# Optimization experiments

Measured on AMD Instinct MI355X. Metric: run time of the kernel, lower is better.

The kernel has to match this reference:

```python
import jax, jax.numpy as jnp
import numpy as np

BLK = 128          # block size for fp8 block-wise scales
FP8_MAX = 448.0    # max representable magnitude of float8_e4m3fn


def _dequant_act(a, s):
    # a: (E, M, K) fp8 values stored in fp32; s: (E, M, K//BLK) per-token 1x128 scales
    E, M, K = a.shape
    nb = K // BLK
    return (a.reshape(E, M, nb, BLK) * s[..., None]).reshape(E, M, K)


def _dequant_w(w, s):
    # w: (E, N, K) fp8 values stored in fp32; s: (E, N//BLK, K//BLK) 128x128 block scales
    E, N, K = w.shape
    return (w.reshape(E, N // BLK, BLK, K // BLK, BLK) * s[:, :, None, :, None]).reshape(E, N, K)


def _fp8_round(x):
    # round-to-fp8(e4m3fn) with straight-through value semantics
    q = x.astype(jnp.float8_e4m3fn).astype(jnp.float32)
    return x + jax.lax.stop_gradient(q - x)


def setup_inputs() -> dict:
    key = jax.random.key(0)
    ks = jax.random.split(key, 8)
    E, N, K, M = 8, 2048, 4096, 1024
    f8 = lambda x: x.astype(jnp.float8_e4m3fn).astype(jnp.float32)
    hidden_states_fp8 = f8(jax.random.normal(ks[0], (E, M, K), dtype=jnp.float32))
    hidden_states_scale = jax.random.uniform(ks[1], (E, M, K // BLK), dtype=jnp.float32, minval=0.01, maxval=1.0)
    masked_m = jax.random.randint(ks[2], (E,), 1, M + 1, dtype=jnp.int32)
    w13_weight_fp8 = f8(jax.random.normal(ks[3], (E, N, K), dtype=jnp.float32))
    w13_weight_scale = jax.random.uniform(ks[4], (E, N // BLK, K // BLK), dtype=jnp.float32, minval=0.01, maxval=1.0)
    w2_weight_fp8 = f8(jax.random.normal(ks[5], (E, K, N // 2), dtype=jnp.float32))
    w2_weight_scale = jax.random.uniform(ks[6], (E, K // BLK, N // 2 // BLK), dtype=jnp.float32, minval=0.01, maxval=1.0)
    return {
        "hidden_states_fp8": hidden_states_fp8,
        "hidden_states_scale": hidden_states_scale,
        "masked_m": masked_m,
        "expected_m": 512,
        "w13_weight_fp8": w13_weight_fp8,
        "w13_weight_scale": w13_weight_scale,
        "w2_weight_fp8": w2_weight_fp8,
        "w2_weight_scale": w2_weight_scale,
    }


def reference(hidden_states_fp8, hidden_states_scale, masked_m, expected_m,
              w13_weight_fp8, w13_weight_scale, w2_weight_fp8, w2_weight_scale):
    E, M, K = hidden_states_fp8.shape
    # per-expert row validity mask (rows >= masked_m[e] are padding)
    mask = jnp.arange(M)[None, :] < masked_m[:, None]            # (E, M)

    # --- grouped GEMM 1: (x @ w13^T) -> bf16, masked by valid rows ---
    a = _dequant_act(hidden_states_fp8, hidden_states_scale)     # (E, M, K)
    w13 = _dequant_w(w13_weight_fp8, w13_weight_scale)           # (E, N, K)
    gateup = jnp.einsum('emk,enk->emn', a, w13)
    gateup = gateup.astype(jnp.bfloat16).astype(jnp.float32)     # gemm emits bf16

    # --- fused SiLU * mul + per-128-block fp8 quantization ---
    gate, up = jnp.split(gateup, 2, axis=-1)                     # (E, M, N/2) each
    x = jax.nn.silu(gate) * up
    x = jnp.where(mask[..., None], x, 0.0)
    N2 = x.shape[-1]
    nb = N2 // BLK
    xb = x.reshape(E, M, nb, BLK)
    amax = jnp.max(jnp.abs(xb), axis=-1)                         # (E, M, nb)
    scale = jnp.maximum(amax, 1e-10) / FP8_MAX
    q = _fp8_round(xb / scale[..., None])                        # fp8-rounded values
    a2 = (q * scale[..., None]).reshape(E, M, N2)                # dequantized for gemm 2

    # --- grouped GEMM 2: (down_input @ w2^T) -> bf16 ---
    w2 = _dequant_w(w2_weight_fp8, w2_weight_scale)              # (E, K, N/2)
    out = jnp.einsum('emn,ekn->emk', a2, w2).astype(jnp.bfloat16)
    out = jnp.where(mask[..., None], out, jnp.bfloat16(0))
    return out
```

## Files before the change

kernel.cpp:

```cpp
#include <hip/hip_runtime.h>
#include <hip/hip_bf16.h>

#define E_  8
#define M_  1024
#define K_  4096
#define N_  2048
#define N2_ 1024

typedef unsigned short u16;
typedef unsigned char  u8;
typedef unsigned int   u32;
typedef long           i64;

typedef __bf16 bf16x8 __attribute__((ext_vector_type(8)));
typedef float  f32x4  __attribute__((ext_vector_type(4)));

union FragU { uint4 u; bf16x8 v; };

__device__ __forceinline__ u16 f2bfu(float f){
  union { __hip_bfloat16 h; u16 u; } c;
  c.h = __float2bfloat16(f);
  return c.u;
}
__device__ __forceinline__ u32 pack2(float a, float b){
  return (u32)f2bfu(a) | ((u32)f2bfu(b) << 16);
}
__device__ __forceinline__ float bf2f(u16 u){
  u32 x = ((u32)u) << 16;
  return __uint_as_float(x);
}
__device__ __forceinline__ float bf16val(float f){
  return bf2f(f2bfu(f));
}
__device__ __forceinline__ float fp8_round(float x){
  float ax = fabsf(x);
  if (ax < 0.015625f){
    return rintf(x * 512.0f) * (1.0f/512.0f);
  }
  u32 u = __float_as_uint(x);
  u32 lsb = (u >> 20) & 1u;
  u += 0x7FFFFu + lsb;
  u &= 0xFFF00000u;
  return __uint_as_float(u);
}
__device__ __forceinline__ u32 f2fp8(float v){
  u32 b = __float_as_uint(v);
  u32 s = (b >> 24) & 0x80u;
  int e = (int)((b >> 23) & 0xffu);
  u32 m = (b >> 20) & 7u;
  if (e >= 121) return s | ((u32)(e - 120) << 3) | m;
  return s | (u32)(fabsf(v) * 512.0f + 0.25f);
}

#define GLD16(g, l) __builtin_amdgcn_global_load_lds( \
    (const __attribute__((address_space(1))) void*)(g), \
    (__attribute__((address_space(3))) void*)(l), 16, 0, 0)

template<bool MASKED>
__global__ __launch_bounds__(256) void conv8_kernel(
    const float* __restrict__ src_, const int* __restrict__ masked_m,
    u8* __restrict__ dst)
{
  const int row = blockIdx.x, e = blockIdx.y;
  if (MASKED && row >= masked_m[e]) return;
  const int t = threadIdx.x;
  const size_t R = (size_t)e*gridDim.x + row;
  const float* s = src_ + R*K_ + t*16;
  const float4 f0 = *reinterpret_cast<const float4*>(s);
  const float4 f1 = *reinterpret_cast<const float4*>(s + 4);
  const float4 f2 = *reinterpret_cast<const float4*>(s + 8);
  const float4 f3 = *reinterpret_cast<const float4*>(s + 12);
  uint4 w;
  w.x = f2fp8(f0.x) | (f2fp8(f0.y)<<8) | (f2fp8(f0.z)<<16) | (f2fp8(f0.w)<<24);
  w.y = f2fp8(f1.x) | (f2fp8(f1.y)<<8) | (f2fp8(f1.z)<<16) | (f2fp8(f1.w)<<24);
  w.z = f2fp8(f2.x) | (f2fp8(f2.y)<<8) | (f2fp8(f2.z)<<16) | (f2fp8(f2.w)<<24);
  w.w = f2fp8(f3.x) | (f2fp8(f3.y)<<8) | (f2fp8(f3.z)<<16) | (f2fp8(f3.w)<<24);
  const int td = (t & ~7) | ((t & 7) ^ (row & 7));
  *reinterpret_cast<uint4*>(dst + R*K_ + td*16) = w;
}

__global__ __launch_bounds__(256, 2) void gemm1_fp8(
    const u8* __restrict__ A8, const float* __restrict__ Ascale,
    const u8* __restrict__ B8, const float* __restrict__ Wscale,
    const int* __restrict__ masked_m, u16* __restrict__ Cu)
{
  const int tn = blockIdx.x, tm = blockIdx.y, e = blockIdx.z;
  const int m0 = tm*128, n0 = tn*128;
  const int me = masked_m[e];
  if (m0 >= me) return;
  const int tid = threadIdx.x;
  const int lane = tid & 63, wid = tid >> 6;

  __shared__ u8 sA[2][128*128];
  __shared__ u8 sB[2][128*128];
  __shared__ float sSa[2][128];

  const size_t rbA = (size_t)e*M_ + m0;
  const size_t rbB = (size_t)e*N_ + n0;

  auto ISSUE = [&](const u8* G, size_t rowbase, int kt, u8* Sbuf){
    #pragma unroll
    for (int q = 0; q < 4; ++q){
      const int ins = wid*4 + q;
      const int r   = ins*8 + (lane >> 3);
      const u8* src = G + (rowbase + r)*K_ + kt*128 + (lane & 7)*16;
      GLD16(src, Sbuf + ins*1024);
    }
  };

  const int wm = wid >> 1, wn = wid & 1;
  const int fr = lane & 15, kg = lane >> 4;

  f32x4 acc[4][4];
  #pragma unroll
  for (int i = 0; i < 4; ++i)
    #pragma unroll
    for (int j = 0; j < 4; ++j)
      acc[i][j] = (f32x4){0.f, 0.f, 0.f, 0.f};

  float rSa = 0.f;
  if (tid < 128) rSa = Ascale[(rbA + tid)*32 + 0];
  ISSUE(A8, rbA, 0, sA[0]);
  ISSUE(B8, rbB, 0, sB[0]);
  if (tid < 128) sSa[0][tid] = rSa;
  asm volatile("s_waitcnt vmcnt(0) lgkmcnt(0)" ::: "memory");
  __builtin_amdgcn_s_barrier();
  __builtin_amdgcn_sched_barrier(0);

  int cur = 0;
  for (int kt = 0; kt < 32; ++kt){
    if (kt + 1 < 32){
      if (tid < 128) rSa = Ascale[(rbA + tid)*32 + kt + 1];
      ISSUE(A8, rbA, kt + 1, sA[cur ^ 1]);
      ISSUE(B8, rbB, kt + 1, sB[cur ^ 1]);
      if (tid < 128) sSa[cur ^ 1][tid] = rSa;
      asm volatile("s_waitcnt vmcnt(8)" ::: "memory");
    } else {
      asm volatile("s_waitcnt vmcnt(0)" ::: "memory");
    }
    __builtin_amdgcn_s_barrier();
    __builtin_amdgcn_sched_barrier(0);

    const float sw = Wscale[((size_t)e*16 + tn)*32 + kt];
    f32x4 blk[4][4];
    #pragma unroll
    for (int ks = 0; ks < 4; ++ks){
      i64 av[4], bv[4];
      #pragma unroll
      for (int i = 0; i < 4; ++i){
        const int r   = wm*64 + i*16 + fr;
        const int c16 = ks*2 + (kg >> 1);
        const int ad  = r*128 + ((c16 ^ (r & 7)) << 4) + ((kg & 1) << 3);
        av[i] = *reinterpret_cast<const i64*>(&sA[cur][ad]);
      }
      #pragma unroll
      for (int j = 0; j < 4; ++j){
        const int r   = wn*64 + j*16 + fr;
        const int c16 = ks*2 + (kg >> 1);
        const int ad  = r*128 + ((c16 ^ (r & 7)) << 4) + ((kg & 1) << 3);
        bv[j] = *reinterpret_cast<const i64*>(&sB[cur][ad]);
      }
      asm volatile("s_waitcnt lgkmcnt(0)" ::: "memory");
      __builtin_amdgcn_sched_barrier(0);
      __builtin_amdgcn_s_setprio(1);
      #pragma unroll
      for (int i = 0; i < 4; ++i)
        #pragma unroll
        for (int j = 0; j < 4; ++j){
          f32x4 cin = (ks == 0) ? (f32x4){0.f,0.f,0.f,0.f} : blk[i][j];
          blk[i][j] = __builtin_amdgcn_mfma_f32_16x16x32_fp8_fp8(av[i], bv[j], cin, 0, 0, 0);
        }
      __builtin_amdgcn_s_setprio(0);
      if (ks == 3){
        #pragma unroll
        for (int i = 0; i < 4; ++i){
          f32x4 sa = *reinterpret_cast<const f32x4*>(&sSa[cur][wm*64 + i*16 + kg*4]);
          sa *= sw;
          #pragma unroll
          for (int j = 0; j < 4; ++j)
            acc[i][j] += sa * blk[i][j];
        }
        asm volatile("s_waitcnt lgkmcnt(0)" ::: "memory");
      }
      __builtin_amdgcn_s_barrier();
    }
    cur ^= 1;
  }

  #pragma unroll
  for (int i = 0; i < 4; ++i){
    #pragma unroll
    for (int j = 0; j < 4; ++j){
      #pragma unroll
      for (int r = 0; r < 4; ++r){
        const int gm = m0 + wm*64 + i*16 + kg*4 + r;
        const int gn = n0 + wn*64 + j*16 + fr;
        if (gm < me) Cu[((size_t)e*M_ + gm)*N_ + gn] = f2bfu(acc[i][j][r]);
      }
    }
  }
}

template<int KD, int ND>
__global__ __launch_bounds__(256, 2) void gemm2_bf16(
    const u16* __restrict__ Abf, const float* __restrict__ Bptr,
    const float* __restrict__ Wscale, const int* __restrict__ masked_m,
    float* __restrict__ Cf)
{
  constexpr int BK  = 64;
  constexpr int KT  = KD / BK;
  constexpr int NKB = KD / 128;
  const int tn = blockIdx.x, tm = blockIdx.y, e = blockIdx.z;
  const int m0 = tm * 128, n0 = tn * 128;
  const int me = masked_m[e];
  const int tid = threadIdx.x;

  if (m0 >= me){
    const uint4 z = make_uint4(0u,0u,0u,0u);
    #pragma unroll
    for (int q = 0; q < 16; ++q){
      int idx = tid + 256*q;
      int r = idx >> 5, c = idx & 31;
      *reinterpret_cast<uint4*>(Cf + ((size_t)e*M_ + m0 + r)*ND + n0 + c*4) = z;
    }
    return;
  }

  __shared__ u16 sA[2][128*64];
  __shared__ u16 sB[2][128*64];

  const int lane = tid & 63, wid = tid >> 6;
  const int rrow = tid >> 3;
  const int kq   = tid & 7;

  float4 rB[8];
  float  sWv = 0.f;

  auto ISSUE_A = [&](int kt, int buf){
    const int k0 = kt * BK;
    #pragma unroll
    for (int q = 0; q < 4; ++q){
      const int ins = wid*4 + q;
      const int r   = ins*8 + (lane >> 3);
      const u16* src = Abf + ((size_t)e*M_ + m0 + r)*KD + k0 + (lane & 7)*8;
      GLD16(src, &sA[buf][ins*512]);
    }
  };
  auto LOAD_B = [&](int kt){
    const int k0 = kt * BK;
    const int kb = k0 >> 7;
    sWv = Wscale[((size_t)e*(ND/128) + tn)*NKB + kb];
    #pragma unroll
    for (int p = 0; p < 4; ++p){
      const int r = p*32 + rrow;
      const float* bp = Bptr + ((size_t)e*ND + n0 + r)*KD + k0 + kq*8;
      rB[2*p]   = *reinterpret_cast<const float4*>(bp);
      rB[2*p+1] = *reinterpret_cast<const float4*>(bp + 4);
    }
  };
  auto WRITE_B = [&](int buf){
    #pragma unroll
    for (int p = 0; p < 4; ++p){
      const int r   = p*32 + rrow;
      const int dst = r*64 + ((kq ^ (r & 7)) * 8);
      uint4 wb;
      wb.x = pack2(rB[2*p].x * sWv,   rB[2*p].y * sWv);
      wb.y = pack2(rB[2*p].z * sWv,   rB[2*p].w * sWv);
      wb.z = pack2(rB[2*p+1].x * sWv, rB[2*p+1].y * sWv);
      wb.w = pack2(rB[2*p+1].z * sWv, rB[2*p+1].w * sWv);
      *reinterpret_cast<uint4*>(&sB[buf][dst]) = wb;
    }
  };

  const int wm = wid >> 1, wn = wid & 1;
  const int fr = lane & 15, kg = lane >> 4;

  f32x4 acc[4][4];
  #pragma unroll
  for (int i = 0; i < 4; ++i)
    #pragma unroll
    for (int j = 0; j < 4; ++j)
      acc[i][j] = (f32x4){0.f, 0.f, 0.f, 0.f};

  auto COMPUTE = [&](int buf){
    #pragma unroll
    for (int ks = 0; ks < 2; ++ks){
      FragU av[4], bv[4];
      #pragma unroll
      for (int i = 0; i < 4; ++i){
        const int r  = wm*64 + i*16 + fr;
        const int ch = (ks*4 + kg) ^ (r & 7);
        av[i].u = *reinterpret_cast<const uint4*>(&sA[buf][r*64 + ch*8]);
      }
      #pragma unroll
      for (int j = 0; j < 4; ++j){
        const int r  = wn*64 + j*16 + fr;
        const int ch = (ks*4 + kg) ^ (r & 7);
        bv[j].u = *reinterpret_cast<const uint4*>(&sB[buf][r*64 + ch*8]);
      }
      #pragma unroll
      for (int i = 0; i < 4; ++i)
        #pragma unroll
        for (int j = 0; j < 4; ++j)
          acc[i][j] = __builtin_amdgcn_mfma_f32_16x16x32_bf16(av[i].v, bv[j].v, acc[i][j], 0, 0, 0);
    }
  };

  ISSUE_A(0, 0);
  LOAD_B(0);
  WRITE_B(0);
  __syncthreads();
  int cur = 0;
  for (int kt = 0; kt < KT; ++kt){
    if (kt + 1 < KT){
      ISSUE_A(kt + 1, cur ^ 1);
      LOAD_B(kt + 1);
    }
    COMPUTE(cur);
    if (kt + 1 < KT) WRITE_B(cur ^ 1);
    __syncthreads();
    cur ^= 1;
  }

  #pragma unroll
  for (int i = 0; i < 4; ++i){
    #pragma unroll
    for (int j = 0; j < 4; ++j){
      #pragma unroll
      for (int r = 0; r < 4; ++r){
        const int gm = m0 + wm*64 + i*16 + kg*4 + r;
        const int gn = n0 + wn*64 + j*16 + fr;
        const float v = (gm < me) ? bf16val(acc[i][j][r]) : 0.0f;
        Cf[((size_t)e*M_ + gm)*ND + gn] = v;
      }
    }
  }
}

__global__ __launch_bounds__(128) void act_quant_kernel(
    const u16* __restrict__ gu, const int* __restrict__ masked_m,
    u16* __restrict__ a2)
{
  const int m = blockIdx.x, e = blockIdx.y;
  if (m >= masked_m[e]) return;
  const int t = threadIdx.x;
  const u16* row = gu + ((size_t)e*M_ + m)*N_;
  uint4 g4 = *reinterpret_cast<const uint4*>(row + t*8);
  uint4 u4 = *reinterpret_cast<const uint4*>(row + N2_ + t*8);
  u32 gp[4] = {g4.x, g4.y, g4.z, g4.w};
  u32 up[4] = {u4.x, u4.y, u4.z, u4.w};

  float x[8];
  #pragma unroll
  for (int w = 0; w < 4; ++w){
    float g0 = bf2f((u16)(gp[w] & 0xffffu));
    float g1 = bf2f((u16)(gp[w] >> 16));
    float u0 = bf2f((u16)(up[w] & 0xffffu));
    float u1 = bf2f((u16)(up[w] >> 16));
    x[2*w]   = g0 / (1.0f + expf(-g0)) * u0;
    x[2*w+1] = g1 / (1.0f + expf(-g1)) * u1;
  }

  float amax = 0.f;
  #pragma unroll
  for (int k = 0; k < 8; ++k) amax = fmaxf(amax, fabsf(x[k]));
  #pragma unroll
  for (int o = 8; o > 0; o >>= 1) amax = fmaxf(amax, __shfl_xor(amax, o, 16));
  const float scale = fmaxf(amax, 1e-10f) / 448.0f;

  u32 hh[4];
  #pragma unroll
  for (int w = 0; w < 4; ++w){
    float d0 = fp8_round(x[2*w]   / scale) * scale;
    float d1 = fp8_round(x[2*w+1] / scale) * scale;
    hh[w] = pack2(d0, d1);
  }
  uint4 o4 = make_uint4(hh[0], hh[1], hh[2], hh[3]);
  const int td = (t & ~7) | ((t & 7) ^ (m & 7));
  *reinterpret_cast<uint4*>(a2 + ((size_t)e*M_ + m)*N2_ + td*8) = o4;
}

extern "C" void kernel_launch(void* const* d_in, const int* in_sizes, int n_in,
                              void* d_out, int out_size, void* d_ws, size_t ws_size,
                              hipStream_t stream)
{
  const float* hs   = (const float*)d_in[0];
  const float* hss  = (const float*)d_in[1];
  const int*   mm   = (const int*)d_in[2];
  const float* w13  = (const float*)d_in[4];
  const float* w13s = (const float*)d_in[5];
  const float* w2   = (const float*)d_in[6];
  const float* w2s  = (const float*)d_in[7];

  u16* gu    = (u16*)d_out;
  u8*  hs8   = (u8*)d_out + (size_t)E_*M_*N_*2;
  u8*  w13_8 = (u8*)d_out + (size_t)E_*M_*N_*2 + (size_t)E_*M_*K_;
  u16* a2    = (u16*)d_ws;

  conv8_kernel<true> <<<dim3(M_, E_), dim3(256), 0, stream>>>(hs,  mm, hs8);
  conv8_kernel<false><<<dim3(N_, E_), dim3(256), 0, stream>>>(w13, mm, w13_8);
  gemm1_fp8<<<dim3(N_/128, M_/128, E_), dim3(256), 0, stream>>>(
      hs8, hss, w13_8, w13s, mm, gu);
  act_quant_kernel<<<dim3(M_, E_), dim3(128), 0, stream>>>(gu, mm, a2);
  gemm2_bf16<N2_, K_><<<dim3(K_/128, M_/128, E_), dim3(256), 0, stream>>>(
      a2, w2, w2s, mm, (float*)d_out);
}
```

Baseline: 311.2 us.

## Pre-pack fp8 operands into MFMA-friendly 64-K slabs with triple-buffered GEMM1 pipeline

```diff
diff --git a/kernel.cpp b/kernel.cpp
--- a/kernel.cpp
+++ b/kernel.cpp
@@ -16,6 +16,7 @@
 typedef float  f32x4  __attribute__((ext_vector_type(4)));
 
 union FragU { uint4 u; bf16x8 v; };
+union U4    { uint4 q; i64 d[2]; };
 
 __device__ __forceinline__ u16 f2bfu(float f){
   union { __hip_bfloat16 h; u16 u; } c;
@@ -56,27 +57,37 @@
     (const __attribute__((address_space(1))) void*)(g), \
     (__attribute__((address_space(3))) void*)(l), 16, 0, 0)
 
-template<bool MASKED>
-__global__ __launch_bounds__(256) void conv8_kernel(
+template<bool MASKED, int R2>
+__global__ __launch_bounds__(256) void conv8p_kernel(
     const float* __restrict__ src_, const int* __restrict__ masked_m,
     u8* __restrict__ dst)
 {
-  const int row = blockIdx.x, e = blockIdx.y;
-  if (MASKED && row >= masked_m[e]) return;
+  const int r = blockIdx.x, e = blockIdx.y;
+  if (MASKED && r >= masked_m[e]) return;
   const int t = threadIdx.x;
-  const size_t R = (size_t)e*gridDim.x + row;
-  const float* s = src_ + R*K_ + t*16;
+  constexpr int R = R2 * 2;
+  const float* s = src_ + ((size_t)e*R + r)*K_ + t*16;
   const float4 f0 = *reinterpret_cast<const float4*>(s);
   const float4 f1 = *reinterpret_cast<const float4*>(s + 4);
   const float4 f2 = *reinterpret_cast<const float4*>(s + 8);
   const float4 f3 = *reinterpret_cast<const float4*>(s + 12);
-  uint4 w;
-  w.x = f2fp8(f0.x) | (f2fp8(f0.y)<<8) | (f2fp8(f0.z)<<16) | (f2fp8(f0.w)<<24);
-  w.y = f2fp8(f1.x) | (f2fp8(f1.y)<<8) | (f2fp8(f1.z)<<16) | (f2fp8(f1.w)<<24);
-  w.z = f2fp8(f2.x) | (f2fp8(f2.y)<<8) | (f2fp8(f2.z)<<16) | (f2fp8(f2.w)<<24);
-  w.w = f2fp8(f3.x) | (f2fp8(f3.y)<<8) | (f2fp8(f3.z)<<16) | (f2fp8(f3.w)<<24);
-  const int td = (t & ~7) | ((t & 7) ^ (row & 7));
-  *reinterpret_cast<uint4*>(dst + R*K_ + td*16) = w;
+  const u32 pA = f2fp8(f0.x) | (f2fp8(f0.y)<<8) | (f2fp8(f0.z)<<16) | (f2fp8(f0.w)<<24);
+  const u32 pB = f2fp8(f1.x) | (f2fp8(f1.y)<<8) | (f2fp8(f1.z)<<16) | (f2fp8(f1.w)<<24);
+  const u32 pC = f2fp8(f2.x) | (f2fp8(f2.y)<<8) | (f2fp8(f2.z)<<16) | (f2fp8(f2.w)<<24);
+  const u32 pD = f2fp8(f3.x) | (f2fp8(f3.y)<<8) | (f2fp8(f3.z)<<16) | (f2fp8(f3.w)<<24);
+
+  const int t64 = t >> 2;
+  const int kk0 = (t & 3) * 16;
+  const int ks  = kk0 >> 5;
+  const int kgA = (kk0 >> 3) & 3;
+  const int u   = r >> 1, par = r & 1;
+  u8* unit = dst + (size_t)e*R*K_ + ((size_t)t64*R2 + u)*128;
+  const int cA = (par*4 + kgA)     ^ (u & 7);
+  const int cB = (par*4 + kgA + 1) ^ (u & 7);
+  uint2 vA; vA.x = pA; vA.y = pB;
+  uint2 vB; vB.x = pC; vB.y = pD;
+  *reinterpret_cast<uint2*>(unit + cA*16 + ks*8) = vA;
+  *reinterpret_cast<uint2*>(unit + cB*16 + ks*8) = vB;
 }
 
 __global__ __launch_bounds__(256, 2) void gemm1_fp8(
@@ -91,100 +102,104 @@
   const int tid = threadIdx.x;
   const int lane = tid & 63, wid = tid >> 6;
 
-  __shared__ u8 sA[2][128*128];
-  __shared__ u8 sB[2][128*128];
-  __shared__ float sSa[2][128];
-
-  const size_t rbA = (size_t)e*M_ + m0;
-  const size_t rbB = (size_t)e*N_ + n0;
-
-  auto ISSUE = [&](const u8* G, size_t rowbase, int kt, u8* Sbuf){
-    #pragma unroll
-    for (int q = 0; q < 4; ++q){
-      const int ins = wid*4 + q;
-      const int r   = ins*8 + (lane >> 3);
-      const u8* src = G + (rowbase + r)*K_ + kt*128 + (lane & 7)*16;
-      GLD16(src, Sbuf + ins*1024);
-    }
+  __shared__ u8 sA3[3][64*128];
+  __shared__ u8 sB3[3][64*128];
+  __shared__ float sSaAll[32][128];
+  __shared__ float sSw[32];
+
+  const u8* gA = A8 + (size_t)e*M_*K_ + (size_t)(m0 >> 1)*128;
+  const u8* gB = B8 + (size_t)e*N_*K_ + (size_t)(n0 >> 1)*128;
+  constexpr size_t strA = (size_t)(M_/2)*128;
+  constexpr size_t strB = (size_t)(N_/2)*128;
+
+  auto ISSUE = [&](int kt, int b){
+    const u8* a = gA + (size_t)kt*strA + (wid*2)*1024 + lane*16;
+    GLD16(a,        &sA3[b][(wid*2  )*1024]);
+    GLD16(a + 1024, &sA3[b][(wid*2+1)*1024]);
+    const u8* bb = gB + (size_t)kt*strB + (wid*2)*1024 + lane*16;
+    GLD16(bb,        &sB3[b][(wid*2  )*1024]);
+    GLD16(bb + 1024, &sB3[b][(wid*2+1)*1024]);
   };
 
   const int wm = wid >> 1, wn = wid & 1;
   const int fr = lane & 15, kg = lane >> 4;
 
+  for (int q = 0; q < 16; ++q){
+    int idx = tid + 256*q;
+    int row = idx & 127, kb = idx >> 7;
+    sSaAll[kb][row] = Ascale[((size_t)e*M_ + m0 + row)*32 + kb];
+  }
+  if (tid < 32) sSw[tid] = Wscale[((size_t)e*16 + tn)*32 + tid];
+  asm volatile("s_waitcnt lgkmcnt(0)" ::: "memory");
+  __builtin_amdgcn_sched_barrier(0);
+  ISSUE(0, 0);
+  ISSUE(1, 1);
+
   f32x4 acc[4][4];
   #pragma unroll
   for (int i = 0; i < 4; ++i)
     #pragma unroll
     for (int j = 0; j < 4; ++j)
       acc[i][j] = (f32x4){0.f, 0.f, 0.f, 0.f};
-
-  float rSa = 0.f;
-  if (tid < 128) rSa = Ascale[(rbA + tid)*32 + 0];
-  ISSUE(A8, rbA, 0, sA[0]);
-  ISSUE(B8, rbB, 0, sB[0]);
-  if (tid < 128) sSa[0][tid] = rSa;
-  asm volatile("s_waitcnt vmcnt(0) lgkmcnt(0)" ::: "memory");
-  __builtin_amdgcn_s_barrier();
-  __builtin_amdgcn_sched_barrier(0);
+  f32x4 blk[4][4];
 
   int cur = 0;
-  for (int kt = 0; kt < 32; ++kt){
-    if (kt + 1 < 32){
-      if (tid < 128) rSa = Ascale[(rbA + tid)*32 + kt + 1];
-      ISSUE(A8, rbA, kt + 1, sA[cur ^ 1]);
-      ISSUE(B8, rbB, kt + 1, sB[cur ^ 1]);
-      if (tid < 128) sSa[cur ^ 1][tid] = rSa;
+  for (int kt = 0; kt < 64; ++kt){
+    if (kt <= 61){
+      int nb = cur + 2; if (nb >= 3) nb -= 3;
+      ISSUE(kt + 2, nb);
       asm volatile("s_waitcnt vmcnt(8)" ::: "memory");
+    } else if (kt == 62){
+      asm volatile("s_waitcnt vmcnt(4)" ::: "memory");
     } else {
       asm volatile("s_waitcnt vmcnt(0)" ::: "memory");
     }
     __builtin_amdgcn_s_barrier();
     __builtin_amdgcn_sched_barrier(0);
 
-    const float sw = Wscale[((size_t)e*16 + tn)*32 + kt];
-    f32x4 blk[4][4];
-    #pragma unroll
-    for (int ks = 0; ks < 4; ++ks){
-      i64 av[4], bv[4];
-      #pragma unroll
-      for (int i = 0; i < 4; ++i){
-        const int r   = wm*64 + i*16 + fr;
-        const int c16 = ks*2 + (kg >> 1);
-        const int ad  = r*128 + ((c16 ^ (r & 7)) << 4) + ((kg & 1) << 3);
-        av[i] = *reinterpret_cast<const i64*>(&sA[cur][ad]);
-      }
-      #pragma unroll
-      for (int j = 0; j < 4; ++j){
-        const int r   = wn*64 + j*16 + fr;
-        const int c16 = ks*2 + (kg >> 1);
-        const int ad  = r*128 + ((c16 ^ (r & 7)) << 4) + ((kg & 1) << 3);
-        bv[j] = *reinterpret_cast<const i64*>(&sB[cur][ad]);
-      }
-      asm volatile("s_waitcnt lgkmcnt(0)" ::: "memory");
-      __builtin_amdgcn_sched_barrier(0);
-      __builtin_amdgcn_s_setprio(1);
+    U4 av[4], bv[4];
+    #pragma unroll
+    for (int i = 0; i < 4; ++i){
+      const int r  = wm*64 + i*16 + fr;
+      const int u  = r >> 1;
+      const int ch = ((r & 1)*4 + kg) ^ (u & 7);
+      av[i].q = *reinterpret_cast<const uint4*>(&sA3[cur][u*128 + ch*16]);
+    }
+    #pragma unroll
+    for (int j = 0; j < 4; ++j){
+      const int r  = wn*64 + j*16 + fr;
+      const int u  = r >> 1;
+      const int ch = ((r & 1)*4 + kg) ^ (u & 7);
+      bv[j].q = *reinterpret_cast<const uint4*>(&sB3[cur][u*128 + ch*16]);
+    }
+    __builtin_amdgcn_s_setprio(1);
+    #pragma unroll
+    for (int ks = 0; ks < 2; ++ks){
+      const bool zero = ((kt & 1) == 0) && (ks == 0);
       #pragma unroll
       for (int i = 0; i < 4; ++i)
         #pragma unroll
         for (int j = 0; j < 4; ++j){
-          f32x4 cin = (ks == 0) ? (f32x4){0.f,0.f,0.f,0.f} : blk[i][j];
-          blk[i][j] = __builtin_amdgcn_mfma_f32_16x16x32_fp8_fp8(av[i], bv[j], cin, 0, 0, 0);
+          f32x4 cin = zero ? (f32x4){0.f,0.f,0.f,0.f} : blk[i][j];
+          blk[i][j] = __builtin_amdgcn_mfma_f32_16x16x32_fp8_fp8(
+                        av[i].d[ks], bv[j].d[ks], cin, 0, 0, 0);
         }
-      __builtin_amdgcn_s_setprio(0);
-      if (ks == 3){
+    }
+    __builtin_amdgcn_s_setprio(0);
+    if (kt & 1){
+      const int kb = kt >> 1;
+      const float sw = sSw[kb];
+      #pragma unroll
+      for (int i = 0; i < 4; ++i){
+        f32x4 sa = *reinterpret_cast<const f32x4*>(&sSaAll[kb][wm*64 + i*16 + kg*4]);
+        sa *= sw;
         #pragma unroll
-        for (int i = 0; i < 4; ++i){
-          f32x4 sa = *reinterpret_cast<const f32x4*>(&sSa[cur][wm*64 + i*16 + kg*4]);
-          sa *= sw;
-          #pragma unroll
-          for (int j = 0; j < 4; ++j)
-            acc[i][j] += sa * blk[i][j];
-        }
-        asm volatile("s_waitcnt lgkmcnt(0)" ::: "memory");
+        for (int j = 0; j < 4; ++j)
+          acc[i][j] += sa * blk[i][j];
       }
-      __builtin_amdgcn_s_barrier();
-    }
-    cur ^= 1;
+    }
+    __builtin_amdgcn_s_barrier();
+    cur = (cur == 2) ? 0 : cur + 1;
   }
 
   #pragma unroll
@@ -397,8 +412,8 @@
   u8*  w13_8 = (u8*)d_out + (size_t)E_*M_*N_*2 + (size_t)E_*M_*K_;
   u16* a2    = (u16*)d_ws;
 
-  conv8_kernel<true> <<<dim3(M_, E_), dim3(256), 0, stream>>>(hs,  mm, hs8);
-  conv8_kernel<false><<<dim3(N_, E_), dim3(256), 0, stream>>>(w13, mm, w13_8);
+  conv8p_kernel<true,  M_/2><<<dim3(M_, E_), dim3(256), 0, stream>>>(hs,  mm, hs8);
+  conv8p_kernel<false, N_/2><<<dim3(N_, E_), dim3(256), 0, stream>>>(w13, mm, w13_8);
   gemm1_fp8<<<dim3(N_/128, M_/128, E_), dim3(256), 0, stream>>>(
       hs8, hss, w13_8, w13s, mm, gu);
   act_quant_kernel<<<dim3(M_, E_), dim3(128), 0, stream>>>(gu, mm, a2);
```

Result: slower. 340.6 us (+9.4%).
